# Optimization experiments

Hardware: AMD Instinct MI355X
Metric: run time of the kernel (lower is better)

## Reference

```python
import jax, jax.numpy as jnp
import numpy as np

CLIP_RATIO = 16.0 / 1000.0
MEAN = (0.0, 0.0, 0.0, 0.0)
STD = (1.0, 1.0, 1.0, 1.0)


def setup_inputs() -> dict:
    key = jax.random.key(0)
    k1, k2, k3, k4, k5 = jax.random.split(key, 5)
    B, N, C = 4, 100000, 80
    logits = jax.random.uniform(k1, (B, N, C), dtype=jnp.float32)
    regress = jax.random.normal(k2, (B, N, 4), dtype=jnp.float32) * 0.5
    confs = jax.random.uniform(k3, (B, N, C), dtype=jnp.float32)
    # valid normalized xyxy anchors: centers in [0,1], sizes in [0.01, 0.3]
    cxy = jax.random.uniform(k4, (N, 2), dtype=jnp.float32)
    wh = jax.random.uniform(k5, (N, 2), dtype=jnp.float32, minval=0.01, maxval=0.3)
    anchors = jnp.concatenate([cxy - wh / 2, cxy + wh / 2], axis=-1)
    return {"logits": logits, "regress": regress, "anchors": anchors, "confs": confs}


def delta2bbox(anchors, deltas, mean=MEAN, std=STD, clip_ratio=CLIP_RATIO):
    # anchors: [N, 4] xyxy, deltas: [B, N, 4] (dx, dy, dw, dh)
    mean = jnp.asarray(mean, dtype=deltas.dtype)
    std = jnp.asarray(std, dtype=deltas.dtype)
    d = deltas * std + mean
    dx, dy = d[..., 0], d[..., 1]
    max_ratio = jnp.abs(jnp.log(jnp.asarray(clip_ratio, dtype=deltas.dtype)))
    dw = jnp.clip(d[..., 2], -max_ratio, max_ratio)
    dh = jnp.clip(d[..., 3], -max_ratio, max_ratio)
    px = (anchors[..., 0] + anchors[..., 2]) * 0.5  # [N]
    py = (anchors[..., 1] + anchors[..., 3]) * 0.5
    pw = anchors[..., 2] - anchors[..., 0]
    ph = anchors[..., 3] - anchors[..., 1]
    gx = px + pw * dx
    gy = py + ph * dy
    gw = pw * jnp.exp(dw)
    gh = ph * jnp.exp(dh)
    return jnp.stack([gx - gw * 0.5, gy - gh * 0.5, gx + gw * 0.5, gy + gh * 0.5], axis=-1)


def reference(logits, regress, anchors, confs):
    # FilterDetection.call with tensorrt=True, valid=False
    scores = logits * confs                      # [B, N, C]
    boxes = delta2bbox(anchors, regress)         # [B, N, 4]
    boxes = jnp.clip(boxes, 0.0, 1.0)
    return (scores, boxes)
```

## Files before the change

### kernel.cpp

```cpp
#include <hip/hip_runtime.h>


#define FD_B 4
#define FD_N 100000
#define FD_C 80

constexpr int SCORES_ELEMS = FD_B * FD_N * FD_C;
constexpr int SCORES_V4    = SCORES_ELEMS / 4;
constexpr int NUM_BOXES    = FD_B * FD_N;
constexpr int TOTAL_WORK   = SCORES_V4 + NUM_BOXES;

#define MAX_RATIO 4.135166556742356f

__global__ __launch_bounds__(256) void fd_kernel(
    const float4* __restrict__ logits,
    const float4* __restrict__ regress,
    const float4* __restrict__ anchors,
    const float4* __restrict__ confs,
    float4* __restrict__ out_scores,
    float4* __restrict__ out_boxes)
{
    int stride = gridDim.x * blockDim.x;
    for (int i = blockIdx.x * blockDim.x + threadIdx.x; i < TOTAL_WORK; i += stride) {
        if (i < SCORES_V4) {
            float4 l = logits[i];
            float4 c = confs[i];
            float4 s;
            s.x = l.x * c.x;
            s.y = l.y * c.y;
            s.z = l.z * c.z;
            s.w = l.w * c.w;
            out_scores[i] = s;
        } else {
            int bi = i - SCORES_V4;
            int n  = bi % FD_N;
            float4 d = regress[bi];
            float4 a = anchors[n];

            float px = (a.x + a.z) * 0.5f;
            float py = (a.y + a.w) * 0.5f;
            float pw = a.z - a.x;
            float ph = a.w - a.y;

            float dw = fminf(fmaxf(d.z, -MAX_RATIO), MAX_RATIO);
            float dh = fminf(fmaxf(d.w, -MAX_RATIO), MAX_RATIO);

            float gx = px + pw * d.x;
            float gy = py + ph * d.y;
            float gw = pw * expf(dw);
            float gh = ph * expf(dh);

            float4 o;
            o.x = gx - gw * 0.5f;
            o.y = gy - gh * 0.5f;
            o.z = gx + gw * 0.5f;
            o.w = gy + gh * 0.5f;

            o.x = fminf(fmaxf(o.x, 0.0f), 1.0f);
            o.y = fminf(fmaxf(o.y, 0.0f), 1.0f);
            o.z = fminf(fmaxf(o.z, 0.0f), 1.0f);
            o.w = fminf(fmaxf(o.w, 0.0f), 1.0f);

            out_boxes[bi] = o;
        }
    }
}

extern "C" void kernel_launch(void* const* d_in, const int* in_sizes, int n_in,
                              void* d_out, int out_size, void* d_ws, size_t ws_size,
                              hipStream_t stream) {
    const float4* logits  = (const float4*)d_in[0];
    const float4* regress = (const float4*)d_in[1];
    const float4* anchors = (const float4*)d_in[2];
    const float4* confs   = (const float4*)d_in[3];

    float* out = (float*)d_out;
    float4* out_scores = (float4*)out;
    float4* out_boxes  = (float4*)(out + SCORES_ELEMS);

    const int block = 256;
    const int grid  = 2048;
    fd_kernel<<<grid, block, 0, stream>>>(logits, regress, anchors, confs,
                                          out_scores, out_boxes);
}
```

Measured before the change: 311.1 us.

## Split grid into score and box blocks, unroll loads, use nontemporal stores

Gives the scores and the boxes their own fixed sets of blocks, sized to the work in each, instead of one grid-stride loop that branches on the index. Each thread now issues four independent float4 loads before computing, to keep more memory requests in flight. Outputs are written with nontemporal stores to avoid polluting the cache. The kernel was already bandwidth-bound, so the gains are likely small, and the block split could leave the box work unbalanced against the scores.

```diff
diff --git a/kernel.cpp b/kernel.cpp
--- a/kernel.cpp
+++ b/kernel.cpp
@@ -8,9 +8,49 @@
 constexpr int SCORES_ELEMS = FD_B * FD_N * FD_C;
 constexpr int SCORES_V4    = SCORES_ELEMS / 4;
 constexpr int NUM_BOXES    = FD_B * FD_N;
-constexpr int TOTAL_WORK   = SCORES_V4 + NUM_BOXES;
+
+constexpr int BLOCK        = 256;
+constexpr int SCORE_BLOCKS = 1953;
+constexpr int BOX_BLOCKS   = 95;
+constexpr int GRID         = SCORE_BLOCKS + BOX_BLOCKS;
 
 #define MAX_RATIO 4.135166556742356f
+
+typedef float vf4 __attribute__((ext_vector_type(4)));
+
+__device__ __forceinline__ void nt_store4(float4 v, float4* p) {
+    vf4 t;
+    t.x = v.x; t.y = v.y; t.z = v.z; t.w = v.w;
+    __builtin_nontemporal_store(t, (vf4*)p);
+}
+
+__device__ __forceinline__ float4 mul4(float4 a, float4 b) {
+    float4 r;
+    r.x = a.x * b.x; r.y = a.y * b.y; r.z = a.z * b.z; r.w = a.w * b.w;
+    return r;
+}
+
+__device__ __forceinline__ float4 box_compute(float4 d, float4 a) {
+    float px = (a.x + a.z) * 0.5f;
+    float py = (a.y + a.w) * 0.5f;
+    float pw = a.z - a.x;
+    float ph = a.w - a.y;
+
+    float dw = fminf(fmaxf(d.z, -MAX_RATIO), MAX_RATIO);
+    float dh = fminf(fmaxf(d.w, -MAX_RATIO), MAX_RATIO);
+
+    float gx = px + pw * d.x;
+    float gy = py + ph * d.y;
+    float gw = pw * expf(dw);
+    float gh = ph * expf(dh);
+
+    float4 o;
+    o.x = fminf(fmaxf(gx - gw * 0.5f, 0.0f), 1.0f);
+    o.y = fminf(fmaxf(gy - gh * 0.5f, 0.0f), 1.0f);
+    o.z = fminf(fmaxf(gx + gw * 0.5f, 0.0f), 1.0f);
+    o.w = fminf(fmaxf(gy + gh * 0.5f, 0.0f), 1.0f);
+    return o;
+}
 
 __global__ __launch_bounds__(256) void fd_kernel(
     const float4* __restrict__ logits,
@@ -20,48 +60,48 @@
     float4* __restrict__ out_scores,
     float4* __restrict__ out_boxes)
 {
-    int stride = gridDim.x * blockDim.x;
-    for (int i = blockIdx.x * blockDim.x + threadIdx.x; i < TOTAL_WORK; i += stride) {
-        if (i < SCORES_V4) {
-            float4 l = logits[i];
-            float4 c = confs[i];
-            float4 s;
-            s.x = l.x * c.x;
-            s.y = l.y * c.y;
-            s.z = l.z * c.z;
-            s.w = l.w * c.w;
-            out_scores[i] = s;
-        } else {
-            int bi = i - SCORES_V4;
-            int n  = bi % FD_N;
-            float4 d = regress[bi];
-            float4 a = anchors[n];
+    if (blockIdx.x < SCORE_BLOCKS) {
+        const int stride = SCORE_BLOCKS * BLOCK;
+        int i = blockIdx.x * BLOCK + threadIdx.x;
 
-            float px = (a.x + a.z) * 0.5f;
-            float py = (a.y + a.w) * 0.5f;
-            float pw = a.z - a.x;
-            float ph = a.w - a.y;
+        for (; i + 3 * stride < SCORES_V4; i += 4 * stride) {
+            float4 l0 = logits[i];
+            float4 l1 = logits[i +     stride];
+            float4 l2 = logits[i + 2 * stride];
+            float4 l3 = logits[i + 3 * stride];
+            float4 c0 = confs[i];
+            float4 c1 = confs[i +     stride];
+            float4 c2 = confs[i + 2 * stride];
+            float4 c3 = confs[i + 3 * stride];
+            nt_store4(mul4(l0, c0), &out_scores[i]);
+            nt_store4(mul4(l1, c1), &out_scores[i +     stride]);
+            nt_store4(mul4(l2, c2), &out_scores[i + 2 * stride]);
+            nt_store4(mul4(l3, c3), &out_scores[i + 3 * stride]);
+        }
+        for (; i < SCORES_V4; i += stride) {
+            nt_store4(mul4(logits[i], confs[i]), &out_scores[i]);
+        }
+    } else {
+        const int stride = BOX_BLOCKS * BLOCK;
+        int bi = (blockIdx.x - SCORE_BLOCKS) * BLOCK + threadIdx.x;
 
-            float dw = fminf(fmaxf(d.z, -MAX_RATIO), MAX_RATIO);
-            float dh = fminf(fmaxf(d.w, -MAX_RATIO), MAX_RATIO);
-
-            float gx = px + pw * d.x;
-            float gy = py + ph * d.y;
-            float gw = pw * expf(dw);
-            float gh = ph * expf(dh);
-
-            float4 o;
-            o.x = gx - gw * 0.5f;
-            o.y = gy - gh * 0.5f;
-            o.z = gx + gw * 0.5f;
-            o.w = gy + gh * 0.5f;
-
-            o.x = fminf(fmaxf(o.x, 0.0f), 1.0f);
-            o.y = fminf(fmaxf(o.y, 0.0f), 1.0f);
-            o.z = fminf(fmaxf(o.z, 0.0f), 1.0f);
-            o.w = fminf(fmaxf(o.w, 0.0f), 1.0f);
-
-            out_boxes[bi] = o;
+        for (; bi + 3 * stride < NUM_BOXES; bi += 4 * stride) {
+            int b0 = bi, b1 = bi + stride, b2 = bi + 2 * stride, b3 = bi + 3 * stride;
+            float4 d0 = regress[b0];
+            float4 d1 = regress[b1];
+            float4 d2 = regress[b2];
+            float4 d3 = regress[b3];
+            float4 a0 = anchors[b0 % FD_N];
+            float4 a1 = anchors[b1 % FD_N];
+            float4 a2 = anchors[b2 % FD_N];
+            float4 a3 = anchors[b3 % FD_N];
+            nt_store4(box_compute(d0, a0), &out_boxes[b0]);
+            nt_store4(box_compute(d1, a1), &out_boxes[b1]);
+            nt_store4(box_compute(d2, a2), &out_boxes[b2]);
+            nt_store4(box_compute(d3, a3), &out_boxes[b3]);
+        }
+        for (; bi < NUM_BOXES; bi += stride) {
+            nt_store4(box_compute(regress[bi], anchors[bi % FD_N]), &out_boxes[bi]);
         }
     }
 }
@@ -78,8 +118,6 @@
     float4* out_scores = (float4*)out;
     float4* out_boxes  = (float4*)(out + SCORES_ELEMS);
 
-    const int block = 256;
-    const int grid  = 2048;
-    fd_kernel<<<grid, block, 0, stream>>>(logits, regress, anchors, confs,
+    fd_kernel<<<GRID, BLOCK, 0, stream>>>(logits, regress, anchors, confs,
                                           out_scores, out_boxes);
 }
```

Result: slower. 327.6 us (+5.3%).
